# Optimization experiments

Measured on AMD Instinct MI355X. Metric: run time of the kernel, lower is better.

The kernel has to match this reference:

```python
import jax, jax.numpy as jnp
import numpy as np

N_A, N_B, N_C = 100000, 60000, 40000
N = N_A + N_B + N_C  # 200000 total nodes after concat
E = 3200000
D_IN = (512, 256, 128)
D = 64  # com_feat_dim == emb_dim


def setup_inputs() -> dict:
    key = jax.random.key(0)
    ks = jax.random.split(key, 16)
    inp = {
        "feat_a": jax.random.normal(ks[0], (N_A, D_IN[0]), jnp.float32),
        "W_a": jax.random.normal(ks[1], (D_IN[0], D), jnp.float32) * 0.05,
        "b_a": jax.random.normal(ks[2], (D,), jnp.float32) * 0.05,
        "feat_b": jax.random.normal(ks[3], (N_B, D_IN[1]), jnp.float32),
        "W_b": jax.random.normal(ks[4], (D_IN[1], D), jnp.float32) * 0.05,
        "b_b": jax.random.normal(ks[5], (D,), jnp.float32) * 0.05,
        "feat_c": jax.random.normal(ks[6], (N_C, D_IN[2]), jnp.float32),
        "W_c": jax.random.normal(ks[7], (D_IN[2], D), jnp.float32) * 0.05,
        "b_c": jax.random.normal(ks[8], (D,), jnp.float32) * 0.05,
        "gcn_W": jax.random.normal(ks[9], (D, D), jnp.float32) * 0.1,
        "gcn_b": jax.random.normal(ks[10], (D,), jnp.float32) * 0.05,
        "edge_weight": jax.random.uniform(ks[11], (E,), jnp.float32),
        "edge_src": jax.random.randint(ks[12], (E,), 0, N, jnp.int32),
        "edge_dst": jax.random.randint(ks[13], (E,), 0, N, jnp.int32),
    }
    return inp


def reference(feat_a, W_a, b_a, feat_b, W_b, b_b, feat_c, W_c, b_c,
              gcn_W, gcn_b, edge_weight, edge_src, edge_dst):
    # Per-type linear encoders + ReLU, then concat over the node axis
    enc = jnp.concatenate([
        jax.nn.relu(feat_a @ W_a + b_a),
        jax.nn.relu(feat_b @ W_b + b_b),
        jax.nn.relu(feat_c @ W_c + b_c),
    ], axis=0)  # [N, D]
    # GraphConvolution: out = spmm(adj, enc @ W + b)
    support = enc @ gcn_W + gcn_b                    # [N, D]
    msg = support[edge_src] * edge_weight[:, None]   # [E, D] irregular gather
    com_emb = jax.ops.segment_sum(msg, edge_dst, num_segments=N)  # [N, D]
    # F.normalize(p=2, dim=1)
    norm = jnp.linalg.norm(com_emb, axis=1, keepdims=True)
    com_emb = com_emb / jnp.maximum(norm, 1e-12)
    return com_emb
```

## Files before the change

kernel.cpp:

```cpp
#include <hip/hip_runtime.h>

#define N_A 100000
#define N_B 60000
#define N_C 40000
#define NTOT 200000
#define NEDGE 3200000
#define D 64


__device__ __forceinline__ void tile_mm64(const float* __restrict__ sA,
                                          const float* __restrict__ sW,
                                          const int nidx[4], int d0,
                                          float acc[4][2])
{
#pragma unroll
    for (int kk = 0; kk < 64; kk += 4) {
        float wl[4], wh[4];
#pragma unroll
        for (int u = 0; u < 4; ++u) {
            wl[u] = sW[(kk + u) * 64 + d0];
            wh[u] = sW[(kk + u) * 64 + d0 + 32];
        }
#pragma unroll
        for (int j = 0; j < 4; ++j) {
            const float4 f = *(const float4*)(sA + nidx[j] * 64 + kk);
            acc[j][0] = fmaf(f.x, wl[0], acc[j][0]);
            acc[j][0] = fmaf(f.y, wl[1], acc[j][0]);
            acc[j][0] = fmaf(f.z, wl[2], acc[j][0]);
            acc[j][0] = fmaf(f.w, wl[3], acc[j][0]);
            acc[j][1] = fmaf(f.x, wh[0], acc[j][1]);
            acc[j][1] = fmaf(f.y, wh[1], acc[j][1]);
            acc[j][1] = fmaf(f.z, wh[2], acc[j][1]);
            acc[j][1] = fmaf(f.w, wh[3], acc[j][1]);
        }
    }
}

template <int K>
__global__ __launch_bounds__(256) void enc_gcn_kernel(
    const float* __restrict__ feat, const float* __restrict__ W,
    const float* __restrict__ bias, const float* __restrict__ gW,
    const float* __restrict__ gb, float* __restrict__ support, int node0)
{
    __shared__ float sW[64 * 64];
    __shared__ float sF[32 * 64];
    __shared__ float sE[32 * 64];

    const int tid = threadIdx.x;
    const int d0  = tid & 31;
    const int h   = (tid >> 5) & 1;
    const int w   = tid >> 6;
    const int blockNode = blockIdx.x * 32;

    int nidx[4];
#pragma unroll
    for (int j = 0; j < 4; ++j) nidx[j] = j * 8 + w * 2 + h;

    float acc[4][2] = {};

    for (int k0 = 0; k0 < K; k0 += 64) {
#pragma unroll
        for (int i = 0; i < 16; ++i) {
            int idx = i * 256 + tid;
            sW[idx] = W[(long long)(k0 + (idx >> 6)) * 64 + (idx & 63)];
        }
#pragma unroll
        for (int i = 0; i < 8; ++i) {
            int idx = i * 256 + tid;
            sF[idx] = feat[(long long)(blockNode + (idx >> 6)) * K + k0 + (idx & 63)];
        }
        __syncthreads();
        tile_mm64(sF, sW, nidx, d0, acc);
        __syncthreads();
    }

    {
        const float b0 = bias[d0], b1 = bias[d0 + 32];
#pragma unroll
        for (int j = 0; j < 4; ++j) {
            sE[nidx[j] * 64 + d0]      = fmaxf(acc[j][0] + b0, 0.f);
            sE[nidx[j] * 64 + d0 + 32] = fmaxf(acc[j][1] + b1, 0.f);
        }
    }
#pragma unroll
    for (int i = 0; i < 16; ++i) {
        int idx = i * 256 + tid;
        sW[idx] = gW[idx];
    }
    __syncthreads();

    float a2[4][2] = {};
    tile_mm64(sE, sW, nidx, d0, a2);

    const float g0 = gb[d0], g1 = gb[d0 + 32];
#pragma unroll
    for (int j = 0; j < 4; ++j) {
        const long long row = (long long)(node0 + blockNode + nidx[j]);
        support[row * 64 + d0]      = a2[j][0] + g0;
        support[row * 64 + d0 + 32] = a2[j][1] + g1;
    }
}

__global__ void zero_kernel(float4* __restrict__ p, long long n4)
{
    long long i  = (long long)blockIdx.x * blockDim.x + threadIdx.x;
    long long st = (long long)gridDim.x * blockDim.x;
    for (; i < n4; i += st) p[i] = float4{0.f, 0.f, 0.f, 0.f};
}

__global__ void scatter_kernel(const float* __restrict__ support,
                               const float* __restrict__ ew,
                               const int* __restrict__ esrc,
                               const int* __restrict__ edst,
                               float* __restrict__ out, int E)
{
    const int d  = threadIdx.x & 63;
    int gw       = blockIdx.x * (blockDim.x >> 6) + (threadIdx.x >> 6);
    const int nw = gridDim.x * (blockDim.x >> 6);
    for (int e = gw; e < E; e += nw) {
        const int   s = esrc[e];
        const int   t = edst[e];
        const float we = ew[e];
        const float v = support[(long long)s * 64 + d] * we;
        atomicAdd(&out[(long long)t * 64 + d], v);
    }
}

__global__ void normalize_kernel(float* __restrict__ out, int N)
{
    const int d   = threadIdx.x & 63;
    const int row = blockIdx.x * (blockDim.x >> 6) + (threadIdx.x >> 6);
    if (row < N) {
        const long long base = (long long)row * 64;
        float x  = out[base + d];
        float ss = x * x;
#pragma unroll
        for (int o = 32; o; o >>= 1) ss += __shfl_xor(ss, o, 64);
        const float nrm = fmaxf(sqrtf(ss), 1e-12f);
        out[base + d] = x / nrm;
    }
}

extern "C" void kernel_launch(void* const* d_in, const int* in_sizes, int n_in,
                              void* d_out, int out_size, void* d_ws, size_t ws_size,
                              hipStream_t stream)
{
    const float* feat_a = (const float*)d_in[0];
    const float* W_a    = (const float*)d_in[1];
    const float* b_a    = (const float*)d_in[2];
    const float* feat_b = (const float*)d_in[3];
    const float* W_b    = (const float*)d_in[4];
    const float* b_b    = (const float*)d_in[5];
    const float* feat_c = (const float*)d_in[6];
    const float* W_c    = (const float*)d_in[7];
    const float* b_c    = (const float*)d_in[8];
    const float* gcn_W  = (const float*)d_in[9];
    const float* gcn_b  = (const float*)d_in[10];
    const float* ew     = (const float*)d_in[11];
    const int*   esrc   = (const int*)d_in[12];
    const int*   edst   = (const int*)d_in[13];

    float* out     = (float*)d_out;
    float* support = (float*)d_ws;

    zero_kernel<<<2048, 256, 0, stream>>>((float4*)out, (long long)NTOT * D / 4);

    enc_gcn_kernel<512><<<N_A / 32, 256, 0, stream>>>(feat_a, W_a, b_a, gcn_W, gcn_b, support, 0);
    enc_gcn_kernel<256><<<N_B / 32, 256, 0, stream>>>(feat_b, W_b, b_b, gcn_W, gcn_b, support, N_A);
    enc_gcn_kernel<128><<<N_C / 32, 256, 0, stream>>>(feat_c, W_c, b_c, gcn_W, gcn_b, support, N_A + N_B);

    scatter_kernel<<<8192, 256, 0, stream>>>(support, ew, esrc, edst, out, NEDGE);

    normalize_kernel<<<NTOT / 4, 256, 0, stream>>>(out, NTOT);
}
```

Before: 1.207 ms.

## Bucket edges by destination and accumulate in LDS; use register-tiled GEMMs

Replaces the fused encoder+GCN kernel with a generic 128-row register-tiled GEMM that runs per type into the output buffer, then a separate GEMM to produce support. Replaces the global atomic scatter with a counting-sort of edges into 256-node destination buckets, so each block accumulates its bucket in LDS and normalizes in place, removing global atomics and the zero and normalize passes. It adds several extra kernel launches and an edge-buffer write/read of 3.2M entries, and falls back to the old path when the workspace is too small.

```diff
diff --git a/kernel.cpp b/kernel.cpp
--- a/kernel.cpp
+++ b/kernel.cpp
@@ -7,97 +7,232 @@
 #define NEDGE 3200000
 #define D 64
 
-
-__device__ __forceinline__ void tile_mm64(const float* __restrict__ sA,
-                                          const float* __restrict__ sW,
-                                          const int nidx[4], int d0,
-                                          float acc[4][2])
-{
-#pragma unroll
-    for (int kk = 0; kk < 64; kk += 4) {
-        float wl[4], wh[4];
-#pragma unroll
-        for (int u = 0; u < 4; ++u) {
-            wl[u] = sW[(kk + u) * 64 + d0];
-            wh[u] = sW[(kk + u) * 64 + d0 + 32];
-        }
-#pragma unroll
-        for (int j = 0; j < 4; ++j) {
-            const float4 f = *(const float4*)(sA + nidx[j] * 64 + kk);
-            acc[j][0] = fmaf(f.x, wl[0], acc[j][0]);
-            acc[j][0] = fmaf(f.y, wl[1], acc[j][0]);
-            acc[j][0] = fmaf(f.z, wl[2], acc[j][0]);
-            acc[j][0] = fmaf(f.w, wl[3], acc[j][0]);
-            acc[j][1] = fmaf(f.x, wh[0], acc[j][1]);
-            acc[j][1] = fmaf(f.y, wh[1], acc[j][1]);
-            acc[j][1] = fmaf(f.z, wh[2], acc[j][1]);
-            acc[j][1] = fmaf(f.w, wh[3], acc[j][1]);
-        }
-    }
-}
-
-template <int K>
-__global__ __launch_bounds__(256) void enc_gcn_kernel(
-    const float* __restrict__ feat, const float* __restrict__ W,
-    const float* __restrict__ bias, const float* __restrict__ gW,
-    const float* __restrict__ gb, float* __restrict__ support, int node0)
-{
-    __shared__ float sW[64 * 64];
-    __shared__ float sF[32 * 64];
-    __shared__ float sE[32 * 64];
+#define NB 782
+
+template <int K, bool RELU>
+__global__ __launch_bounds__(128) void gemm128_kernel(
+    const float* __restrict__ X, const float* __restrict__ W,
+    const float* __restrict__ bias, float* __restrict__ Y,
+    int Nn, int node0out)
+{
+    __shared__ float sF[32][132];
+    __shared__ float sW[32 * 64];
 
     const int tid = threadIdx.x;
-    const int d0  = tid & 31;
-    const int h   = (tid >> 5) & 1;
     const int w   = tid >> 6;
-    const int blockNode = blockIdx.x * 32;
-
-    int nidx[4];
-#pragma unroll
-    for (int j = 0; j < 4; ++j) nidx[j] = j * 8 + w * 2 + h;
-
-    float acc[4][2] = {};
-
-    for (int k0 = 0; k0 < K; k0 += 64) {
-#pragma unroll
-        for (int i = 0; i < 16; ++i) {
-            int idx = i * 256 + tid;
-            sW[idx] = W[(long long)(k0 + (idx >> 6)) * 64 + (idx & 63)];
-        }
-#pragma unroll
-        for (int i = 0; i < 8; ++i) {
-            int idx = i * 256 + tid;
-            sF[idx] = feat[(long long)(blockNode + (idx >> 6)) * K + k0 + (idx & 63)];
-        }
+    const int l   = tid & 63;
+    const int l5  = l >> 5;
+    const int l31 = l & 31;
+    const int tn  = tid >> 3;
+    const int td  = tid & 7;
+    const int n0  = tn * 8;
+    const int d0  = td * 8;
+    const int bn  = blockIdx.x * 128;
+
+    float  acc[8][8] = {};
+    float4 pf[8];
+    float4 pw[4];
+
+#define LOAD_F(k0_)                                                          \
+    _Pragma("unroll")                                                        \
+    for (int p = 0; p < 8; ++p) {                                            \
+        const int n  = l31 + 32 * (p & 3);                                   \
+        const int tk = l5 + 2 * (p >> 2) + 4 * w;                            \
+        const int gn = bn + n;                                               \
+        pf[p] = (gn < Nn)                                                    \
+            ? *(const float4*)(X + (long long)gn * K + (k0_) + tk * 4)       \
+            : make_float4(0.f, 0.f, 0.f, 0.f);                               \
+    }
+#define LOAD_W(k0_)                                                          \
+    {                                                                        \
+        const float4* gw = (const float4*)(W + (long long)(k0_) * 64);       \
+        _Pragma("unroll")                                                    \
+        for (int c = 0; c < 4; ++c) pw[c] = gw[c * 128 + tid];               \
+    }
+
+    LOAD_F(0)
+    LOAD_W(0)
+
+    for (int k0 = 0; k0 < K; k0 += 32) {
         __syncthreads();
-        tile_mm64(sF, sW, nidx, d0, acc);
+#pragma unroll
+        for (int p = 0; p < 8; ++p) {
+            const int n  = l31 + 32 * (p & 3);
+            const int tk = l5 + 2 * (p >> 2) + 4 * w;
+            sF[tk * 4 + 0][n] = pf[p].x;
+            sF[tk * 4 + 1][n] = pf[p].y;
+            sF[tk * 4 + 2][n] = pf[p].z;
+            sF[tk * 4 + 3][n] = pf[p].w;
+        }
+#pragma unroll
+        for (int c = 0; c < 4; ++c) ((float4*)sW)[c * 128 + tid] = pw[c];
         __syncthreads();
-    }
-
-    {
-        const float b0 = bias[d0], b1 = bias[d0 + 32];
-#pragma unroll
-        for (int j = 0; j < 4; ++j) {
-            sE[nidx[j] * 64 + d0]      = fmaxf(acc[j][0] + b0, 0.f);
-            sE[nidx[j] * 64 + d0 + 32] = fmaxf(acc[j][1] + b1, 0.f);
-        }
-    }
-#pragma unroll
-    for (int i = 0; i < 16; ++i) {
-        int idx = i * 256 + tid;
-        sW[idx] = gW[idx];
-    }
-    __syncthreads();
-
-    float a2[4][2] = {};
-    tile_mm64(sE, sW, nidx, d0, a2);
-
-    const float g0 = gb[d0], g1 = gb[d0 + 32];
-#pragma unroll
-    for (int j = 0; j < 4; ++j) {
-        const long long row = (long long)(node0 + blockNode + nidx[j]);
-        support[row * 64 + d0]      = a2[j][0] + g0;
-        support[row * 64 + d0 + 32] = a2[j][1] + g1;
+        if (k0 + 32 < K) { LOAD_F(k0 + 32) LOAD_W(k0 + 32) }
+
+#pragma unroll 4
+        for (int kk = 0; kk < 32; ++kk) {
+            const float4 f0 = *(const float4*)(&sF[kk][n0]);
+            const float4 f1 = *(const float4*)(&sF[kk][n0 + 4]);
+            const float4 w0 = *(const float4*)(sW + kk * 64 + d0);
+            const float4 w1 = *(const float4*)(sW + kk * 64 + d0 + 4);
+            const float fv[8] = { f0.x, f0.y, f0.z, f0.w, f1.x, f1.y, f1.z, f1.w };
+            const float wv[8] = { w0.x, w0.y, w0.z, w0.w, w1.x, w1.y, w1.z, w1.w };
+#pragma unroll
+            for (int j = 0; j < 8; ++j)
+#pragma unroll
+                for (int i = 0; i < 8; ++i)
+                    acc[j][i] = fmaf(fv[j], wv[i], acc[j][i]);
+        }
+    }
+#undef LOAD_F
+#undef LOAD_W
+
+    float bv[8];
+    *(float4*)&bv[0] = *(const float4*)(bias + d0);
+    *(float4*)&bv[4] = *(const float4*)(bias + d0 + 4);
+#pragma unroll
+    for (int j = 0; j < 8; ++j) {
+        const int gn = bn + n0 + j;
+        if (gn < Nn) {
+            float o[8];
+#pragma unroll
+            for (int i = 0; i < 8; ++i) {
+                o[i] = acc[j][i] + bv[i];
+                if (RELU) o[i] = fmaxf(o[i], 0.f);
+            }
+            float* yp = Y + (long long)(node0out + gn) * 64 + d0;
+            *(float4*)(yp)     = *(float4*)&o[0];
+            *(float4*)(yp + 4) = *(float4*)&o[4];
+        }
+    }
+}
+
+__global__ void zero_ints(int* __restrict__ p, int n)
+{
+    int i = blockIdx.x * blockDim.x + threadIdx.x;
+    if (i < n) p[i] = 0;
+}
+
+__global__ __launch_bounds__(256) void count_kernel(const int* __restrict__ edst,
+                                                    int* __restrict__ gcount, int E)
+{
+    __shared__ int lh[NB];
+    for (int i = threadIdx.x; i < NB; i += 256) lh[i] = 0;
+    __syncthreads();
+    int i  = blockIdx.x * 256 + threadIdx.x;
+    int st = gridDim.x * 256;
+    for (; i < E; i += st) atomicAdd(&lh[edst[i] >> 8], 1);
+    __syncthreads();
+    for (int b = threadIdx.x; b < NB; b += 256)
+        if (lh[b]) atomicAdd(&gcount[b], lh[b]);
+}
+
+__global__ __launch_bounds__(1024) void scan_kernel(const int* __restrict__ gcount,
+                                                    int* __restrict__ bstart,
+                                                    int* __restrict__ gcursor, int nb)
+{
+    const int t = threadIdx.x, lane = t & 63, wid = t >> 6;
+    int v = (t < nb) ? gcount[t] : 0;
+    int x = v;
+#pragma unroll
+    for (int o = 1; o < 64; o <<= 1) {
+        int y = __shfl_up(x, o, 64);
+        if (lane >= o) x += y;
+    }
+    __shared__ int wsum[16];
+    if (lane == 63) wsum[wid] = x;
+    __syncthreads();
+    if (t == 0) {
+        int run = 0;
+#pragma unroll
+        for (int i = 0; i < 16; ++i) { int s = wsum[i]; wsum[i] = run; run += s; }
+    }
+    __syncthreads();
+    const int excl = x - v + wsum[wid];
+    if (t < nb) { bstart[t] = excl; gcursor[t] = excl; }
+    if (t == nb - 1) bstart[nb] = excl + v;
+}
+
+__global__ __launch_bounds__(256) void bucket_scatter(const int* __restrict__ esrc,
+                                                      const int* __restrict__ edst,
+                                                      const float* __restrict__ ew,
+                                                      int* __restrict__ gcursor,
+                                                      uint2* __restrict__ ebuf, int E)
+{
+    __shared__ int lh[NB];
+    __shared__ int lbase[NB];
+    const int G = gridDim.x;
+    const long long e0 = (long long)E * blockIdx.x / G;
+    const long long e1 = (long long)E * (blockIdx.x + 1) / G;
+
+    for (int i = threadIdx.x; i < NB; i += 256) lh[i] = 0;
+    __syncthreads();
+    for (long long e = e0 + threadIdx.x; e < e1; e += 256)
+        atomicAdd(&lh[edst[e] >> 8], 1);
+    __syncthreads();
+    for (int b = threadIdx.x; b < NB; b += 256) {
+        const int c = lh[b];
+        lbase[b] = c ? atomicAdd(&gcursor[b], c) : 0;
+    }
+    __syncthreads();
+    for (int i = threadIdx.x; i < NB; i += 256) lh[i] = 0;
+    __syncthreads();
+    for (long long e = e0 + threadIdx.x; e < e1; e += 256) {
+        const int dst  = edst[e];
+        const int b    = dst >> 8;
+        const int off  = atomicAdd(&lh[b], 1);
+        const unsigned pack = ((unsigned)(dst & 255) << 18) | (unsigned)esrc[e];
+        ebuf[lbase[b] + off] = make_uint2(pack, __float_as_uint(ew[e]));
+    }
+}
+
+__global__ __launch_bounds__(256) void bucket_gather(const float* __restrict__ support,
+                                                     const uint2* __restrict__ ebuf,
+                                                     const int* __restrict__ bstart,
+                                                     float* __restrict__ out)
+{
+    __shared__ float sAcc[256 * 64];
+    const int tid = threadIdx.x, lane = tid & 63, wid = tid >> 6;
+    const int b = blockIdx.x;
+#pragma unroll
+    for (int i = 0; i < 16; ++i)
+        *(float4*)(&sAcc[(i * 256 + tid) * 4]) = make_float4(0.f, 0.f, 0.f, 0.f);
+    __syncthreads();
+
+    const int start = bstart[b], end = bstart[b + 1];
+    for (int base = start + (wid << 2); base < end; base += 16) {
+        const int m = end - base;
+        if (m >= 4) {
+            const uint2 c0 = ebuf[base], c1 = ebuf[base + 1];
+            const uint2 c2 = ebuf[base + 2], c3 = ebuf[base + 3];
+            const float v0 = support[(long long)(c0.x & 0x3FFFF) * 64 + lane];
+            const float v1 = support[(long long)(c1.x & 0x3FFFF) * 64 + lane];
+            const float v2 = support[(long long)(c2.x & 0x3FFFF) * 64 + lane];
+            const float v3 = support[(long long)(c3.x & 0x3FFFF) * 64 + lane];
+            atomicAdd(&sAcc[(c0.x >> 18) * 64 + lane], v0 * __uint_as_float(c0.y));
+            atomicAdd(&sAcc[(c1.x >> 18) * 64 + lane], v1 * __uint_as_float(c1.y));
+            atomicAdd(&sAcc[(c2.x >> 18) * 64 + lane], v2 * __uint_as_float(c2.y));
+            atomicAdd(&sAcc[(c3.x >> 18) * 64 + lane], v3 * __uint_as_float(c3.y));
+        } else {
+            for (int j = 0; j < m; ++j) {
+                const uint2 c = ebuf[base + j];
+                const float v = support[(long long)(c.x & 0x3FFFF) * 64 + lane];
+                atomicAdd(&sAcc[(c.x >> 18) * 64 + lane], v * __uint_as_float(c.y));
+            }
+        }
+    }
+    __syncthreads();
+
+    for (int r = wid; r < 256; r += 4) {
+        const int gn = b * 256 + r;
+        if (gn < NTOT) {
+            const float x = sAcc[r * 64 + lane];
+            float ss = x * x;
+#pragma unroll
+            for (int o = 32; o; o >>= 1) ss += __shfl_xor(ss, o, 64);
+            const float nrm = fmaxf(sqrtf(ss), 1e-12f);
+            out[(long long)gn * 64 + lane] = x / nrm;
+        }
     }
 }
 
@@ -118,11 +253,8 @@
     int gw       = blockIdx.x * (blockDim.x >> 6) + (threadIdx.x >> 6);
     const int nw = gridDim.x * (blockDim.x >> 6);
     for (int e = gw; e < E; e += nw) {
-        const int   s = esrc[e];
-        const int   t = edst[e];
-        const float we = ew[e];
-        const float v = support[(long long)s * 64 + d] * we;
-        atomicAdd(&out[(long long)t * 64 + d], v);
+        atomicAdd(&out[(long long)edst[e] * 64 + d],
+                  support[(long long)esrc[e] * 64 + d] * ew[e]);
     }
 }
 
@@ -136,8 +268,7 @@
         float ss = x * x;
 #pragma unroll
         for (int o = 32; o; o >>= 1) ss += __shfl_xor(ss, o, 64);
-        const float nrm = fmaxf(sqrtf(ss), 1e-12f);
-        out[base + d] = x / nrm;
+        out[base + d] = x / fmaxf(sqrtf(ss), 1e-12f);
     }
 }
 
@@ -160,16 +291,37 @@
     const int*   esrc   = (const int*)d_in[12];
     const int*   edst   = (const int*)d_in[13];
 
-    float* out     = (float*)d_out;
-    float* support = (float*)d_ws;
-
-    zero_kernel<<<2048, 256, 0, stream>>>((float4*)out, (long long)NTOT * D / 4);
-
-    enc_gcn_kernel<512><<<N_A / 32, 256, 0, stream>>>(feat_a, W_a, b_a, gcn_W, gcn_b, support, 0);
-    enc_gcn_kernel<256><<<N_B / 32, 256, 0, stream>>>(feat_b, W_b, b_b, gcn_W, gcn_b, support, N_A);
-    enc_gcn_kernel<128><<<N_C / 32, 256, 0, stream>>>(feat_c, W_c, b_c, gcn_W, gcn_b, support, N_A + N_B);
-
-    scatter_kernel<<<8192, 256, 0, stream>>>(support, ew, esrc, edst, out, NEDGE);
-
-    normalize_kernel<<<NTOT / 4, 256, 0, stream>>>(out, NTOT);
-}
+    float* out = (float*)d_out;
+
+    char* ws = (char*)d_ws;
+    const size_t off_support = 0;
+    const size_t off_ebuf    = off_support + (size_t)NTOT * D * 4;
+    const size_t off_gcount  = off_ebuf + (size_t)NEDGE * 8;
+    const size_t off_bstart  = off_gcount + 4096;
+    const size_t off_gcursor = off_bstart + 4096;
+    const size_t need        = off_gcursor + 4096;
+
+    float* support = (float*)(ws + off_support);
+
+    gemm128_kernel<512, true ><<<(N_A  + 127) / 128, 128, 0, stream>>>(feat_a, W_a, b_a, out, N_A, 0);
+    gemm128_kernel<256, true ><<<(N_B  + 127) / 128, 128, 0, stream>>>(feat_b, W_b, b_b, out, N_B, N_A);
+    gemm128_kernel<128, true ><<<(N_C  + 127) / 128, 128, 0, stream>>>(feat_c, W_c, b_c, out, N_C, N_A + N_B);
+    gemm128_kernel< 64, false><<<(NTOT + 127) / 128, 128, 0, stream>>>(out, gcn_W, gcn_b, support, NTOT, 0);
+
+    if (ws_size >= need) {
+        uint2* ebuf    = (uint2*)(ws + off_ebuf);
+        int*   gcount  = (int*)(ws + off_gcount);
+        int*   bstart  = (int*)(ws + off_bstart);
+        int*   gcursor = (int*)(ws + off_gcursor);
+
+        zero_ints<<<(NB + 255) / 256, 256, 0, stream>>>(gcount, NB);
+        count_kernel<<<1024, 256, 0, stream>>>(edst, gcount, NEDGE);
+        scan_kernel<<<1, 1024, 0, stream>>>(gcount, bstart, gcursor, NB);
+        bucket_scatter<<<1024, 256, 0, stream>>>(esrc, edst, ew, gcursor, ebuf, NEDGE);
+        bucket_gather<<<NB, 256, 0, stream>>>(support, ebuf, bstart, out);
+    } else {
+        zero_kernel<<<2048, 256, 0, stream>>>((float4*)out, (long long)NTOT * D / 4);
+        scatter_kernel<<<8192, 256, 0, stream>>>(support, ew, esrc, edst, out, NEDGE);
+        normalize_kernel<<<NTOT / 4, 256, 0, stream>>>(out, NTOT);
+    }
+}
```

Result: slower. 2.037 ms (+68.9%).
